# Kernel tuning notes

Measured on AMD Instinct MI355X. Metric: run time of the kernel, lower is better.

Reference implementation:

```python
import jax, jax.numpy as jnp
import numpy as np

THETA = 10000.0


def apply_rope(x, positions, theta=THETA):
    # x: [B, H, N, D], positions: [1, N] or [B, N]
    D = x.shape[-1]
    inv_freq = 1.0 / (theta ** (jnp.arange(0, D, 2, dtype=jnp.float32) / D))  # [D/2]
    ang = positions.astype(jnp.float32)[:, None, :, None] * inv_freq  # [B_or_1, 1, N, D/2]
    cos, sin = jnp.cos(ang), jnp.sin(ang)
    x1 = x[..., 0::2]
    x2 = x[..., 1::2]
    r1 = x1 * cos - x2 * sin
    r2 = x1 * sin + x2 * cos
    # interleave back to [..., D]
    return jnp.stack([r1, r2], axis=-1).reshape(x.shape)


def setup_inputs() -> dict:
    key = jax.random.key(0)
    ks = jax.random.split(key, 5)
    B, N, d_model = 2, 2048, 1024
    s = 1.0 / np.sqrt(d_model)
    return {
        "x": jax.random.normal(ks[0], (B, N, d_model), dtype=jnp.float32),
        "Wq": jax.random.normal(ks[1], (d_model, d_model), dtype=jnp.float32) * s,
        "Wk": jax.random.normal(ks[2], (d_model, d_model), dtype=jnp.float32) * s,
        "Wv": jax.random.normal(ks[3], (d_model, d_model), dtype=jnp.float32) * s,
        "Wo": jax.random.normal(ks[4], (d_model, d_model), dtype=jnp.float32) * s,
        "token_positions": jnp.arange(N, dtype=jnp.int32)[None, :],
    }


def reference(x, Wq, Wk, Wv, Wo, token_positions):
    B, N, d_model = x.shape
    H = 16
    D = d_model // H
    # projections: out = x @ W.T  (einsum '... i, j i -> ... j')
    def proj(W):
        y = jnp.einsum('bni,ji->bnj', x, W)
        return y.reshape(B, N, H, D).transpose(0, 2, 1, 3)  # [B,H,N,D]
    q, k, v = proj(Wq), proj(Wk), proj(Wv)
    q = apply_rope(q, token_positions)
    k = apply_rope(k, token_positions)
    scale = 1.0 / jnp.sqrt(jnp.asarray(D, dtype=x.dtype))
    scores = jnp.einsum('bhid,bhjd->bhij', q, k) * scale  # [B,H,N,N]
    causal = jnp.tril(jnp.ones((N, N), dtype=bool))
    scores = jnp.where(causal[None, None], scores, -jnp.inf)
    w = jax.nn.softmax(scores, axis=-1)
    o = jnp.einsum('bhij,bhjd->bhid', w, v)  # [B,H,N,D]
    o = o.transpose(0, 2, 1, 3).reshape(B, N, d_model)
    return jnp.einsum('bni,ji->bnj', o, Wo)
```

## Files before the change

kernel.cpp:

```cpp
#include <hip/hip_runtime.h>

#define DMODEL 1024
#define NSEQ   2048
#define BSZ    2
#define NH     16
#define HD     64
#define MROWS  (BSZ*NSEQ)

using short8 = __attribute__((ext_vector_type(8))) short;
using f32x4  = __attribute__((ext_vector_type(4))) float;

__device__ __forceinline__ short f2b(float f) {
  unsigned u = __builtin_bit_cast(unsigned, f);
  u += 0x7fffu + ((u >> 16) & 1u);
  return (short)(u >> 16);
}

__device__ __forceinline__ void load_lds16(const void* g, void* l) {
  __builtin_amdgcn_global_load_lds((const __attribute__((address_space(1))) unsigned int*)g,
                                   (__attribute__((address_space(3))) unsigned int*)l,
                                   16, 0, 0);
}

__global__ void cvt_all(const float* __restrict__ x,  const float* __restrict__ Wq,
                        const float* __restrict__ Wk, const float* __restrict__ Wv,
                        const float* __restrict__ Wo, const int* __restrict__ pos,
                        short* __restrict__ xb,  short* __restrict__ wqb,
                        short* __restrict__ wkb, short* __restrict__ wvb,
                        short* __restrict__ wob, float* __restrict__ cs) {
  const int NX  = (BSZ * NSEQ * DMODEL) / 4;
  const int NW  = (DMODEL * DMODEL) / 4;
  const int NCV = NX + 4 * NW;
  const int TOT = NCV + NSEQ * 32;
  for (int i = blockIdx.x * blockDim.x + threadIdx.x; i < TOT; i += gridDim.x * blockDim.x) {
    if (i < NCV) {
      const float* src; short* dst; int off;
      if (i < NX) { src = x; dst = xb; off = i; }
      else {
        int j = i - NX; int s = j >> 18; off = j & (NW - 1);
        src = (s == 0) ? Wq : (s == 1) ? Wk : (s == 2) ? Wv : Wo;
        dst = (s == 0) ? wqb : (s == 1) ? wkb : (s == 2) ? wvb : wob;
      }
      float4 v = reinterpret_cast<const float4*>(src)[off];
      short4 r;
      r.x = f2b(v.x); r.y = f2b(v.y); r.z = f2b(v.z); r.w = f2b(v.w);
      reinterpret_cast<short4*>(dst)[off] = r;
    } else {
      int idx = i - NCV;
      int n = idx >> 5, p = idx & 31;
      float inv = powf(10000.0f, -(float)(2 * p) / 64.0f);
      float ang = (float)pos[n] * inv;
      cs[idx * 2]     = cosf(ang);
      cs[idx * 2 + 1] = sinf(ang);
    }
  }
}

__global__ __launch_bounds__(512, 1) void gemm_qkv3(
    const short* __restrict__ xb,
    const short* __restrict__ wq, const short* __restrict__ wk, const short* __restrict__ wv,
    const float* __restrict__ cs,
    short* __restrict__ qb, short* __restrict__ kb, short* __restrict__ vt) {
  __shared__ short Al[2][128 * 64];
  __shared__ short Bl[2][3][128 * 64];

  const int t   = threadIdx.x;
  const int l   = t & 63;
  const int wid = t >> 6;
  const int wr  = (wid >> 2) * 64;
  const int wc  = (wid & 3) * 32;

  const int id = blockIdx.x;
  const int bx = id & 31;
  const int np = id >> 5;
  const int arow0 = bx * 128;
  const int bcol0 = np * 128;

  const int tr = t >> 3;
  const int c8 = (t & 7) ^ ((t >> 3) & 7);
  const short* W3[3] = {wq, wk, wv};

  auto STAGE = [&](int kt, int buf) {
#pragma unroll
    for (int h = 0; h < 2; ++h)
      load_lds16(xb + (size_t)(arow0 + h * 64 + tr) * DMODEL + kt * 64 + c8 * 8,
                 &Al[buf][h * 4096 + wid * 512]);
#pragma unroll
    for (int p = 0; p < 3; ++p)
#pragma unroll
      for (int h = 0; h < 2; ++h)
        load_lds16(W3[p] + (size_t)(bcol0 + h * 64 + tr) * DMODEL + kt * 64 + c8 * 8,
                   &Bl[buf][p][h * 4096 + wid * 512]);
  };

  f32x4 acc[3][4][2];
#pragma unroll
  for (int p = 0; p < 3; ++p)
#pragma unroll
    for (int mi = 0; mi < 4; ++mi)
#pragma unroll
      for (int ni = 0; ni < 2; ++ni) acc[p][mi][ni] = f32x4{0.f, 0.f, 0.f, 0.f};

  const int lr  = l & 15;
  const int lcb = (l >> 4) << 4;

  STAGE(0, 0);
  int cur = 0;

  for (int kt = 0; kt < DMODEL / 64; ++kt) {
    if (kt + 1 < DMODEL / 64) {
      STAGE(kt + 1, cur ^ 1);
      asm volatile("s_waitcnt vmcnt(8)" ::: "memory");
    } else {
      asm volatile("s_waitcnt vmcnt(0)" ::: "memory");
    }
    asm volatile("s_barrier" ::: "memory");

    const char* Ab = reinterpret_cast<const char*>(&Al[cur][0]);
#pragma unroll
    for (int ks = 0; ks < 2; ++ks) {
      const int cb = ks * 64 + lcb;
      short8 af[4];
#pragma unroll
      for (int mi = 0; mi < 4; ++mi) {
        int r = wr + mi * 16 + lr;
        af[mi] = *reinterpret_cast<const short8*>(Ab + r * 128 + (cb ^ ((r & 7) << 4)));
      }
#pragma unroll
      for (int p = 0; p < 3; ++p) {
        const char* Bb = reinterpret_cast<const char*>(&Bl[cur][p][0]);
        short8 bf[2];
#pragma unroll
        for (int ni = 0; ni < 2; ++ni) {
          int r = wc + ni * 16 + lr;
          bf[ni] = *reinterpret_cast<const short8*>(Bb + r * 128 + (cb ^ ((r & 7) << 4)));
        }
#pragma unroll
        for (int mi = 0; mi < 4; ++mi)
#pragma unroll
          for (int ni = 0; ni < 2; ++ni)
            acc[p][mi][ni] = __builtin_amdgcn_mfma_f32_16x16x32_bf16(af[mi], bf[ni], acc[p][mi][ni], 0, 0, 0);
      }
    }
    asm volatile("s_barrier" ::: "memory");
    cur ^= 1;
  }

#pragma unroll
  for (int p = 0; p < 3; ++p) {
#pragma unroll
    for (int mi = 0; mi < 4; ++mi) {
#pragma unroll
      for (int ni = 0; ni < 2; ++ni) {
#pragma unroll
        for (int r = 0; r < 4; ++r) {
          float v = acc[p][mi][ni][r];
          int m = arow0 + wr + mi * 16 + ((l >> 4) << 2) + r;
          int j = bcol0 + wc + ni * 16 + (l & 15);
          int n = m & (NSEQ - 1);
          int b = m >> 11;
          int h = j >> 6, d = j & 63, pp = d >> 1;
          float pv = __shfl_xor(v, 1);
          if (p < 2) {
            float c = cs[(n * 32 + pp) * 2];
            float s = cs[(n * 32 + pp) * 2 + 1];
            float res = (d & 1) ? (pv * s + v * c) : (v * c - pv * s);
            if (p == 0) res *= 0.180336880f;
            short* dst = (p == 0) ? qb : kb;
            dst[(((size_t)(b * NH + h)) * NSEQ + n) * HD + d] = f2b(res);
          } else {
            vt[(((size_t)(b * NH + h)) * HD + d) * NSEQ + n] = f2b(v);
          }
        }
      }
    }
  }
}

__device__ __forceinline__ void gemm_core(const short* __restrict__ A,
                                          const short* __restrict__ Bw,
                                          int arow0, int bcol0,
                                          short* As, short* Bs,
                                          f32x4 (&acc)[4][4]) {
  const int t = threadIdx.x;
  const int l = t & 63;
  const int w = t >> 6;
  const int wr = (w >> 1) * 64;
  const int wc = (w & 1) * 64;
  const int srow = t >> 3;
  const int c8   = (t & 7) ^ (srow & 7);

#pragma unroll
  for (int mi = 0; mi < 4; ++mi)
#pragma unroll
    for (int ni = 0; ni < 4; ++ni) acc[mi][ni] = f32x4{0.f, 0.f, 0.f, 0.f};

  auto STAGE = [&](int kt, int buf) {
#pragma unroll
    for (int is = 0; is < 4; ++is) {
      int row = srow + is * 32;
      load_lds16(A  + (size_t)(arow0 + row) * DMODEL + kt * 64 + c8 * 8,
                 As + buf * 8192 + w * 512 + is * 2048);
      load_lds16(Bw + (size_t)(bcol0 + row) * DMODEL + kt * 64 + c8 * 8,
                 Bs + buf * 8192 + w * 512 + is * 2048);
    }
  };

  STAGE(0, 0);
  int cur = 0;

  for (int kt = 0; kt < DMODEL / 64; ++kt) {
    if (kt + 1 < DMODEL / 64) {
      STAGE(kt + 1, cur ^ 1);
      asm volatile("s_waitcnt vmcnt(8)" ::: "memory");
    } else {
      asm volatile("s_waitcnt vmcnt(0)" ::: "memory");
    }
    asm volatile("s_barrier" ::: "memory");

    const char* Ab = reinterpret_cast<const char*>(As + cur * 8192);
    const char* Bb = reinterpret_cast<const char*>(Bs + cur * 8192);
#pragma unroll
    for (int ks = 0; ks < 2; ++ks) {
      short8 af[4], bf[4];
      const int cb = ks * 64 + ((l >> 4) * 16);
#pragma unroll
      for (int mi = 0; mi < 4; ++mi) {
        int rr = wr + mi * 16 + (l & 15);
        af[mi] = *reinterpret_cast<const short8*>(Ab + rr * 128 + (cb ^ ((rr & 7) << 4)));
      }
#pragma unroll
      for (int ni = 0; ni < 4; ++ni) {
        int rr = wc + ni * 16 + (l & 15);
        bf[ni] = *reinterpret_cast<const short8*>(Bb + rr * 128 + (cb ^ ((rr & 7) << 4)));
      }
#pragma unroll
      for (int mi = 0; mi < 4; ++mi)
#pragma unroll
        for (int ni = 0; ni < 4; ++ni)
          acc[mi][ni] = __builtin_amdgcn_mfma_f32_16x16x32_bf16(af[mi], bf[ni], acc[mi][ni], 0, 0, 0);
    }
    asm volatile("s_barrier" ::: "memory");
    cur ^= 1;
  }
}

__global__ __launch_bounds__(256) void gemm_out(
    const short* __restrict__ ob, const short* __restrict__ wo, float* __restrict__ out) {
  __shared__ short As[2 * 128 * 64];
  __shared__ short Bs[2 * 128 * 64];
  const int t = threadIdx.x;
  const int l = t & 63;
  const int w = t >> 6;
  const int wr = (w >> 1) * 64;
  const int wc = (w & 1) * 64;
  const int arow0 = blockIdx.x * 128;
  const int bcol0 = blockIdx.y * 128;

  f32x4 acc[4][4];
  gemm_core(ob, wo, arow0, bcol0, As, Bs, acc);

#pragma unroll
  for (int mi = 0; mi < 4; ++mi) {
#pragma unroll
    for (int ni = 0; ni < 4; ++ni) {
#pragma unroll
      for (int r = 0; r < 4; ++r) {
        int m = arow0 + wr + mi * 16 + ((l >> 4) << 2) + r;
        int j = bcol0 + wc + ni * 16 + (l & 15);
        out[(size_t)m * DMODEL + j] = acc[mi][ni][r];
      }
    }
  }
}

__global__ __launch_bounds__(256) void attn(
    const short* __restrict__ qb, const short* __restrict__ kb,
    const short* __restrict__ vt, short* __restrict__ ob) {
  __shared__ short Ks[2 * 64 * 64];
  __shared__ short Vs[2 * 64 * 64];
  __shared__ short Ps[4][16 * 64];
  const int t = threadIdx.x;
  const int l = t & 63;
  const int w = t >> 6;
  const int id  = blockIdx.x;
  const int xcd = id & 7;
  const int j0g = id >> 3;
  const int bh  = xcd + 8 * (j0g >> 4);
  const int qy  = j0g & 15;
  const short* Q  = qb + (size_t)bh * NSEQ * HD;
  const short* Kg = kb + (size_t)bh * NSEQ * HD;
  const short* Vg = vt + (size_t)bh * HD * NSEQ;
  const int b = bh >> 4, h = bh & 15;

  const int srow = t >> 3;
  const int c8   = (t & 7) ^ (srow & 7);
  const int irow = (l >> 4) << 2;
  const short8 ones = {(short)0x3F80, (short)0x3F80, (short)0x3F80, (short)0x3F80,
                       (short)0x3F80, (short)0x3F80, (short)0x3F80, (short)0x3F80};

  auto STAGEA = [&](int tile, int buf) {
    int j0 = tile * 64;
#pragma unroll
    for (int is = 0; is < 2; ++is) {
      int row = srow + is * 32;
      load_lds16(Kg + (size_t)(j0 + row) * HD + c8 * 8, Ks + buf * 4096 + w * 512 + is * 2048);
      load_lds16(Vg + (size_t)row * NSEQ + j0 + c8 * 8, Vs + buf * 4096 + w * 512 + is * 2048);
    }
  };

  int cur = 0;
  for (int pass = 0; pass < 2; ++pass) {
    const int qt = pass ? (31 - qy) : qy;
    const int q0 = qt * 64;

    STAGEA(0, cur);

    short8 qf[2];
    {
      int qrow = q0 + w * 16 + (l & 15);
#pragma unroll
      for (int ks = 0; ks < 2; ++ks)
        qf[ks] = *reinterpret_cast<const short8*>(Q + (size_t)qrow * HD + ks * 32 + (l >> 4) * 8);
    }

    f32x4 ao[4];
#pragma unroll
    for (int dt = 0; dt < 4; ++dt) ao[dt] = f32x4{0.f, 0.f, 0.f, 0.f};
    f32x4 accl = f32x4{0.f, 0.f, 0.f, 0.f};

    for (int tile = 0; tile <= qt; ++tile) {
      if (tile < qt) {
        STAGEA(tile + 1, cur ^ 1);
        asm volatile("s_waitcnt vmcnt(4)" ::: "memory");
      } else {
        asm volatile("s_waitcnt vmcnt(0)" ::: "memory");
      }
      asm volatile("s_barrier" ::: "memory");

      const char* Kb = reinterpret_cast<const char*>(Ks + cur * 4096);
      const char* Vb = reinterpret_cast<const char*>(Vs + cur * 4096);

      f32x4 sc[4];
#pragma unroll
      for (int jt = 0; jt < 4; ++jt) sc[jt] = f32x4{0.f, 0.f, 0.f, 0.f};
#pragma unroll
      for (int ks = 0; ks < 2; ++ks) {
        const int cb = ks * 64 + ((l >> 4) * 16);
#pragma unroll
        for (int jt = 0; jt < 4; ++jt) {
          int kr = jt * 16 + (l & 15);
          short8 kf = *reinterpret_cast<const short8*>(Kb + kr * 128 + (cb ^ ((kr & 7) << 4)));
          sc[jt] = __builtin_amdgcn_mfma_f32_16x16x32_bf16(qf[ks], kf, sc[jt], 0, 0, 0);
        }
      }

      if (tile == qt) {
#pragma unroll
        for (int jt = 0; jt < 4; ++jt)
#pragma unroll
          for (int r = 0; r < 4; ++r) {
            int i_rel = w * 16 + irow + r;
            int jj = jt * 16 + (l & 15);
            if (jj > i_rel) sc[jt][r] = -1e30f;
          }
      }

#pragma unroll
      for (int jt = 0; jt < 4; ++jt) {
#pragma unroll
        for (int r = 0; r < 4; ++r) {
          float p = __builtin_amdgcn_exp2f(sc[jt][r]);
          int i = irow + r;
          int jj = jt * 16 + (l & 15);
          Ps[w][i * 64 + (jj ^ ((i & 7) << 3))] = f2b(p);
        }
      }

#pragma unroll
      for (int ks2 = 0; ks2 < 2; ++ks2) {
        const int cb = ks2 * 64 + ((l >> 4) * 16);
        int pr = l & 15;
        short8 pf = *reinterpret_cast<const short8*>(
            reinterpret_cast<const char*>(Ps[w]) + pr * 128 + (cb ^ ((pr & 7) << 4)));
        accl = __builtin_amdgcn_mfma_f32_16x16x32_bf16(pf, ones, accl, 0, 0, 0);
#pragma unroll
        for (int dt = 0; dt < 4; ++dt) {
          int vr = dt * 16 + (l & 15);
          short8 vf = *reinterpret_cast<const short8*>(Vb + vr * 128 + (cb ^ ((vr & 7) << 4)));
          ao[dt] = __builtin_amdgcn_mfma_f32_16x16x32_bf16(pf, vf, ao[dt], 0, 0, 0);
        }
      }
      asm volatile("s_barrier" ::: "memory");
      cur ^= 1;
    }

#pragma unroll
    for (int dt = 0; dt < 4; ++dt) {
#pragma unroll
      for (int r = 0; r < 4; ++r) {
        int n = q0 + w * 16 + irow + r;
        int col = h * 64 + dt * 16 + (l & 15);
        ob[((size_t)b * NSEQ + n) * DMODEL + col] = f2b(ao[dt][r] / accl[r]);
      }
    }
  }
}

extern "C" void kernel_launch(void* const* d_in, const int* in_sizes, int n_in,
                              void* d_out, int out_size, void* d_ws, size_t ws_size,
                              hipStream_t stream) {
  const float* x  = (const float*)d_in[0];
  const float* Wq = (const float*)d_in[1];
  const float* Wk = (const float*)d_in[2];
  const float* Wv = (const float*)d_in[3];
  const float* Wo = (const float*)d_in[4];
  const int*   pos = (const int*)d_in[5];
  float* out = (float*)d_out;
  char* ws = (char*)d_ws;

  short* xb  = (short*)(ws);
  short* wqb = (short*)(ws + ((size_t)8  << 20));
  short* wkb = (short*)(ws + ((size_t)10 << 20));
  short* wvb = (short*)(ws + ((size_t)12 << 20));
  short* wob = (short*)(ws + ((size_t)14 << 20));
  short* qb  = (short*)(ws + ((size_t)16 << 20));
  short* kb  = (short*)(ws + ((size_t)24 << 20));
  short* vt  = (short*)(ws + ((size_t)32 << 20));
  short* ob  = (short*)(ws + ((size_t)40 << 20));
  float* cs  = (float*)(ws + ((size_t)48 << 20));

  cvt_all<<<2048, 256, 0, stream>>>(x, Wq, Wk, Wv, Wo, pos, xb, wqb, wkb, wvb, wob, cs);
  gemm_qkv3<<<256, 512, 0, stream>>>(xb, wqb, wkb, wvb, cs, qb, kb, vt);
  attn<<<512, 256, 0, stream>>>(qb, kb, vt, ob);
  gemm_out<<<dim3(32, 8), 256, 0, stream>>>(ob, wob, out);
}
```

Before: 110.8 us.

## Widen attention query tile to 128 rows with 8 waves sharing K/V tiles

The attention kernel now uses 512-thread blocks, each handling a 128-row query tile with eight waves. Each K/V tile staged in LDS is reused by twice as many query rows, and the grid is halved to 256 blocks. The causal mask now uses global indices over the last two key tiles. The P conversion to bf16 switches from round-to-nearest to plain truncation, which is cheaper but slightly less accurate. The trade-offs are fewer blocks (256 on a large GPU) and more work wasted on masked tiles in the diagonal region.

```diff
diff --git a/kernel.cpp b/kernel.cpp
--- a/kernel.cpp
+++ b/kernel.cpp
@@ -274,45 +274,41 @@
   }
 }
 
-__global__ __launch_bounds__(256) void attn(
+__global__ __launch_bounds__(512, 1) void attn(
     const short* __restrict__ qb, const short* __restrict__ kb,
     const short* __restrict__ vt, short* __restrict__ ob) {
-  __shared__ short Ks[2 * 64 * 64];
-  __shared__ short Vs[2 * 64 * 64];
-  __shared__ short Ps[4][16 * 64];
+  __shared__ short Ks[2][64 * 64];
+  __shared__ short Vs[2][64 * 64];
+  __shared__ short Ps[8][16 * 64];
   const int t = threadIdx.x;
   const int l = t & 63;
   const int w = t >> 6;
   const int id  = blockIdx.x;
   const int xcd = id & 7;
-  const int j0g = id >> 3;
-  const int bh  = xcd + 8 * (j0g >> 4);
-  const int qy  = j0g & 15;
+  const int bh  = xcd + 8 * (id >> 6);
+  const int qy  = (id >> 3) & 7;
   const short* Q  = qb + (size_t)bh * NSEQ * HD;
   const short* Kg = kb + (size_t)bh * NSEQ * HD;
   const short* Vg = vt + (size_t)bh * HD * NSEQ;
   const int b = bh >> 4, h = bh & 15;
 
-  const int srow = t >> 3;
-  const int c8   = (t & 7) ^ (srow & 7);
+  const int tr = t >> 3;
+  const int c8 = (t & 7) ^ ((t >> 3) & 7);
   const int irow = (l >> 4) << 2;
   const short8 ones = {(short)0x3F80, (short)0x3F80, (short)0x3F80, (short)0x3F80,
                        (short)0x3F80, (short)0x3F80, (short)0x3F80, (short)0x3F80};
 
   auto STAGEA = [&](int tile, int buf) {
     int j0 = tile * 64;
-#pragma unroll
-    for (int is = 0; is < 2; ++is) {
-      int row = srow + is * 32;
-      load_lds16(Kg + (size_t)(j0 + row) * HD + c8 * 8, Ks + buf * 4096 + w * 512 + is * 2048);
-      load_lds16(Vg + (size_t)row * NSEQ + j0 + c8 * 8, Vs + buf * 4096 + w * 512 + is * 2048);
-    }
+    load_lds16(Kg + (size_t)(j0 + tr) * HD + c8 * 8, &Ks[buf][w * 512]);
+    load_lds16(Vg + (size_t)tr * NSEQ + j0 + c8 * 8, &Vs[buf][w * 512]);
   };
 
   int cur = 0;
   for (int pass = 0; pass < 2; ++pass) {
-    const int qt = pass ? (31 - qy) : qy;
-    const int q0 = qt * 64;
+    const int qt = pass ? (15 - qy) : qy;
+    const int q0 = qt * 128;
+    const int nt = 2 * qt + 2;
 
     STAGEA(0, cur);
 
@@ -329,17 +325,17 @@
     for (int dt = 0; dt < 4; ++dt) ao[dt] = f32x4{0.f, 0.f, 0.f, 0.f};
     f32x4 accl = f32x4{0.f, 0.f, 0.f, 0.f};
 
-    for (int tile = 0; tile <= qt; ++tile) {
-      if (tile < qt) {
+    for (int tile = 0; tile < nt; ++tile) {
+      if (tile + 1 < nt) {
         STAGEA(tile + 1, cur ^ 1);
-        asm volatile("s_waitcnt vmcnt(4)" ::: "memory");
+        asm volatile("s_waitcnt vmcnt(2)" ::: "memory");
       } else {
         asm volatile("s_waitcnt vmcnt(0)" ::: "memory");
       }
       asm volatile("s_barrier" ::: "memory");
 
-      const char* Kb = reinterpret_cast<const char*>(Ks + cur * 4096);
-      const char* Vb = reinterpret_cast<const char*>(Vs + cur * 4096);
+      const char* Kb = reinterpret_cast<const char*>(&Ks[cur][0]);
+      const char* Vb = reinterpret_cast<const char*>(&Vs[cur][0]);
 
       f32x4 sc[4];
 #pragma unroll
@@ -355,14 +351,15 @@
         }
       }
 
-      if (tile == qt) {
+      if (tile >= 2 * qt) {
+        const int j0 = tile * 64;
 #pragma unroll
         for (int jt = 0; jt < 4; ++jt)
 #pragma unroll
           for (int r = 0; r < 4; ++r) {
-            int i_rel = w * 16 + irow + r;
-            int jj = jt * 16 + (l & 15);
-            if (jj > i_rel) sc[jt][r] = -1e30f;
+            int i_g = q0 + w * 16 + irow + r;
+            int j_g = j0 + jt * 16 + (l & 15);
+            if (j_g > i_g) sc[jt][r] = -1e30f;
           }
       }
 
@@ -373,7 +370,8 @@
           float p = __builtin_amdgcn_exp2f(sc[jt][r]);
           int i = irow + r;
           int jj = jt * 16 + (l & 15);
-          Ps[w][i * 64 + (jj ^ ((i & 7) << 3))] = f2b(p);
+          Ps[w][i * 64 + (jj ^ ((i & 7) << 3))] =
+              (short)(__builtin_bit_cast(unsigned, p) >> 16);
         }
       }
 
@@ -382,7 +380,7 @@
         const int cb = ks2 * 64 + ((l >> 4) * 16);
         int pr = l & 15;
         short8 pf = *reinterpret_cast<const short8*>(
-            reinterpret_cast<const char*>(Ps[w]) + pr * 128 + (cb ^ ((pr & 7) << 4)));
+            reinterpret_cast<const char*>(&Ps[w][0]) + pr * 128 + (cb ^ ((pr & 7) << 4)));
         accl = __builtin_amdgcn_mfma_f32_16x16x32_bf16(pf, ones, accl, 0, 0, 0);
 #pragma unroll
         for (int dt = 0; dt < 4; ++dt) {
@@ -432,6 +430,6 @@
 
   cvt_all<<<2048, 256, 0, stream>>>(x, Wq, Wk, Wv, Wo, pos, xb, wqb, wkb, wvb, wob, cs);
   gemm_qkv3<<<256, 512, 0, stream>>>(xb, wqb, wkb, wvb, cs, qb, kb, vt);
-  attn<<<512, 256, 0, stream>>>(qb, kb, vt, ob);
+  attn<<<256, 512, 0, stream>>>(qb, kb, vt, ob);
   gemm_out<<<dim3(32, 8), 256, 0, stream>>>(ob, wob, out);
 }
```

After: 105.2 us. -5.1%, faster.
